# Kernel optimization log

Hardware: AMD Instinct MI355X
Metric: run time of the kernel (lower is better)

Reference implementation:

```python
import jax, jax.numpy as jnp
import numpy as np

B, N, D, E, K, C = 64, 32, 384, 8, 8, 1000  # batch, tokens, dim, experts, capacity, classes
KD = K * D   # expert_dims = 3072
ND = N * D   # 12288

def _gelu(v):
    return jax.nn.gelu(v, approximate=False)  # torch nn.GELU default = exact erf

def setup_inputs() -> dict:
    key = jax.random.key(0)
    ks = jax.random.split(key, 16)
    s = 0.02
    f = jnp.float32
    return {
        "x": jax.random.normal(ks[0], (B, N, D), f),
        "expert_emb": jax.random.normal(ks[1], (E, D), f) * s,
        "w1": jax.random.normal(ks[2], (E, KD, KD), f) * s,
        "b1": jnp.zeros((E, KD), f),
        "w2": jax.random.normal(ks[3], (E, KD, KD), f) * s,
        "b2": jnp.zeros((E, KD), f),
        "sw_w1": jax.random.normal(ks[4], (ND, ND), f) * s,
        "sw_b1": jnp.zeros((ND,), f),
        "sw_w2": jax.random.normal(ks[5], (ND, E), f) * s,
        "sw_b2": jnp.zeros((E,), f),
        "ch_w1": jax.random.normal(ks[6], (KD, KD), f) * s,
        "ch_b1": jnp.zeros((KD,), f),
        "ch_w2": jax.random.normal(ks[7], (KD, C), f) * s,
        "ch_b2": jnp.zeros((C,), f),
    }

def reference(x, expert_emb, w1, b1, w2, b2, sw_w1, sw_b1, sw_w2, sw_b2, ch_w1, ch_b1, ch_w2, ch_b2):
    # Router: scores (B, E, N), softmax over tokens, expert-choice top-k
    S = jax.nn.softmax(jnp.einsum('bnd,ed->ben', x, expert_emb), axis=2)
    G, I = jax.lax.top_k(S, K)  # (B, E, K); G is unused downstream (matches original)
    # Gather selected tokens per expert: (B, E, K, D)
    sel = x[jnp.arange(B)[:, None, None], I]
    sel = jnp.transpose(sel, (1, 0, 2, 3)).reshape(E, B, KD)  # e b (k d)
    # Per-expert MLP as grouped GEMM
    h = _gelu(jnp.einsum('ebi,eio->ebo', sel, w1) + b1[:, None, :])
    er = jnp.einsum('ebi,eio->ebo', h, w2) + b2[:, None, :]   # (E, B, KD)
    er = jnp.transpose(er, (1, 0, 2))                          # (B, E, KD)
    # Weighted combine: weights from Mlp over flattened input + softmax over experts
    xf = x.reshape(B, ND)
    w = jax.nn.softmax(_gelu(xf @ sw_w1 + sw_b1) @ sw_w2 + sw_b2, axis=1)  # (B, E)
    ws = jnp.einsum('bek,be->bk', er, w)                       # (B, KD)
    # Classification head
    return _gelu(ws @ ch_w1 + ch_b1) @ ch_w2 + ch_b2           # (B, C)
```

## Files before the change

kernel.cpp:

```cpp
#include <hip/hip_runtime.h>
#include <hip/hip_bf16.h>

using short8 = __attribute__((ext_vector_type(8))) short;
using f32x4  = __attribute__((ext_vector_type(4))) float;

typedef const __attribute__((address_space(1))) void* gvp;
typedef __attribute__((address_space(3))) void* lvp;

#define NB   64
#define NTOK 32
#define DD   384
#define NE   8
#define TK   8
#define NC   1000
#define KD   3072
#define ND   12288

__device__ __forceinline__ float gelu_f(float x) {
  return 0.5f * x * (1.0f + erff(x * 0.70710678118654752440f));
}

__device__ __forceinline__ unsigned short f2bf(float f) {
  unsigned u = __float_as_uint(f);
  u += 0x7fffu + ((u >> 16) & 1u);
  return (unsigned short)(u >> 16);
}

__global__ __launch_bounds__(256) void routing_kernel(
    const float* __restrict__ x, const float* __restrict__ emb,
    unsigned short* __restrict__ sel, unsigned short* __restrict__ xb)
{
  __shared__ float xs[NTOK][DD + 1];
  __shared__ float es[NE][DD + 1];
  __shared__ float lg[NE][NTOK];
  __shared__ int   Is[NE][TK];
  const int b = blockIdx.x, tid = threadIdx.x;

  for (int i = tid; i < NTOK * DD; i += 256) xs[i / DD][i % DD] = x[(size_t)b * ND + i];
  for (int i = tid; i < NE * DD;   i += 256) es[i / DD][i % DD] = emb[i];
  __syncthreads();

  {
    const int e = tid >> 5, n = tid & 31;
    float s = 0.f;
    for (int d = 0; d < DD; ++d) s += xs[n][d] * es[e][d];
    lg[e][n] = s;
  }
  __syncthreads();

  if (tid < NE) {
    const int e = tid;
    for (int k = 0; k < TK; ++k) {
      float best = lg[e][0]; int bi = 0;
      for (int n = 1; n < NTOK; ++n) { float v = lg[e][n]; if (v > best) { best = v; bi = n; } }
      Is[e][k] = bi;
      lg[e][bi] = -INFINITY;
    }
  }
  __syncthreads();

  for (int i = tid; i < NE * KD; i += 256) {
    const int e = i / KD, r = i % KD, k = r / DD, d = r % DD;
    const int n = Is[e][k];
    sel[((size_t)e * NB + b) * KD + r] = f2bf(xs[n][d]);
  }
  for (int i = tid; i < ND; i += 256) xb[(size_t)b * ND + i] = f2bf(xs[i / DD][i % DD]);
}

__device__ __forceinline__ void gemm_rt_body(
    const unsigned short* __restrict__ Ab, const float* __restrict__ Wz,
    float* __restrict__ op, const int K, const int N, const int NSTEP,
    const int n0, const int wv, const int lane, float* __restrict__ lw)
{
  const int srow = wv * 8 + (lane >> 5);
  const int scol = (((lane & 31) * 4) - wv * 8) & 127;
  const float* gsrc = Wz + (size_t)srow * N + n0 + scol;
  float* lbase = lw + wv * 1024 + lane * 4;

  auto stage = [&](int bf, int st) {
    const float* g = gsrc + (size_t)st * 32 * N;
    float* l = lbase + bf * 4096;
    #pragma unroll
    for (int r = 0; r < 4; ++r)
      __builtin_amdgcn_global_load_lds((gvp)(g + (size_t)(r * 2) * N),
                                       (lvp)(l + r * 256), 16, 0, 0);
  };

  const int ln = lane & 15, q = lane >> 4, g8 = q * 8;
  const unsigned short* ap = Ab + (size_t)ln * K + g8;
  const int colp0 = (wv * 32 +      ln + g8) & 127;
  const int colp1 = (wv * 32 + 16 + ln + g8) & 127;

  f32x4 acc[4][2];
  #pragma unroll
  for (int mt = 0; mt < 4; ++mt) {
    acc[mt][0] = (f32x4){0.f, 0.f, 0.f, 0.f};
    acc[mt][1] = (f32x4){0.f, 0.f, 0.f, 0.f};
  }

  stage(0, 0);
  for (int st = 0; st < NSTEP; ++st) {
    const int bf = st & 1;
    __syncthreads();
    if (st + 1 < NSTEP) stage(bf ^ 1, st + 1);

    const float* lb = lw + bf * 4096;
    union { short8 v; unsigned short u[8]; } pb0, pb1;
    #pragma unroll
    for (int j = 0; j < 8; ++j) {
      pb0.u[j] = f2bf(lb[(g8 + j) * 128 + colp0]);
      pb1.u[j] = f2bf(lb[(g8 + j) * 128 + colp1]);
    }
    #pragma unroll
    for (int mt = 0; mt < 4; ++mt) {
      const short8 afr = *reinterpret_cast<const short8*>(ap + (size_t)mt * 16 * K + st * 32);
      acc[mt][0] = __builtin_amdgcn_mfma_f32_16x16x32_bf16(afr, pb0.v, acc[mt][0], 0, 0, 0);
      acc[mt][1] = __builtin_amdgcn_mfma_f32_16x16x32_bf16(afr, pb1.v, acc[mt][1], 0, 0, 0);
    }
  }

  #pragma unroll
  for (int mt = 0; mt < 4; ++mt)
    #pragma unroll
    for (int s = 0; s < 2; ++s) {
      const int col = n0 + wv * 32 + s * 16 + ln;
      #pragma unroll
      for (int r = 0; r < 4; ++r)
        op[(size_t)(mt * 16 + q * 4 + r) * N + col] = acc[mt][s][r];
    }
}

template<int PHASE>
__global__ __launch_bounds__(256) void dual_gemm(
    const unsigned short* __restrict__ EA, const float* __restrict__ EW,
    float* __restrict__ EO,
    const unsigned short* __restrict__ xb, const float* __restrict__ sww1,
    float* __restrict__ tpt)
{
  __shared__ float lw[2][4096];
  const int t = threadIdx.x, wv = t >> 6, lane = t & 63;
  const int bid = blockIdx.x;
  const int grp = bid >> 1, rem = bid & 1;

  if (rem == 0) {
    const int idx = grp;
    const int z = idx & 1, bt = (idx >> 1) & 7, nx = idx >> 4;
    constexpr int KCH = KD / 2;
    gemm_rt_body(EA + (size_t)bt * 64 * KD + (size_t)z * KCH,
                 EW + (size_t)bt * KD * KD + (size_t)z * KCH * KD,
                 EO + ((size_t)z * NE + bt) * 64 * KD,
                 KD, KD, KCH / 32, nx * 128, wv, lane, &lw[0][0]);
  } else {
    const int idx = grp;
    const int z = PHASE * 4 + (idx & 3), nx = idx >> 2;
    constexpr int KCH = ND / 8;
    gemm_rt_body(xb + (size_t)z * KCH,
                 sww1 + (size_t)z * KCH * ND,
                 tpt + (size_t)z * 64 * ND,
                 ND, ND, KCH / 32, nx * 128, wv, lane, &lw[0][0]);
  }
}

template<int K, int N, int SPLIT, bool NGUARD>
__global__ __launch_bounds__(256) void gemm2(
    const unsigned short* __restrict__ A, const float* __restrict__ W,
    float* __restrict__ outp, const int nbatch)
{
  constexpr int KCH = K / SPLIT;
  constexpr int NSTEP = KCH / 32;
  __shared__ float lw[2][4096];

  const int t = threadIdx.x;
  const int wv = t >> 6, lane = t & 63;
  const int n0 = blockIdx.x * 128;
  const int bt = blockIdx.y, z = blockIdx.z;

  const unsigned short* Ab = A + (size_t)bt * 64 * K + (size_t)z * KCH;
  const float*          Wb = W + (size_t)bt * (size_t)K * N;

  const int srow = wv * 8 + (lane >> 5);
  const int scol = (((lane & 31) * 4) - wv * 8) & 127;
  const float* gsrc   = Wb + (size_t)(z * KCH + srow) * N + n0 + scol;
  const float* glimit = Wb + (size_t)K * N - 4;
  float* lbase = &lw[0][0] + wv * 1024 + lane * 4;

  auto stage = [&](int bf, int st) {
    const float* g = gsrc + (size_t)st * 32 * N;
    float* l = lbase + bf * 4096;
    #pragma unroll
    for (int r = 0; r < 4; ++r) {
      const float* gp = g + (size_t)(r * 2) * N;
      if (NGUARD && gp > glimit) gp = glimit;
      __builtin_amdgcn_global_load_lds((gvp)gp, (lvp)(l + r * 256), 16, 0, 0);
    }
  };

  const int ln = lane & 15, q = lane >> 4, g8 = q * 8;
  const unsigned short* ap = Ab + (size_t)ln * K + g8;
  const int colp0 = (wv * 32 +      ln + g8) & 127;
  const int colp1 = (wv * 32 + 16 + ln + g8) & 127;

  f32x4 acc[4][2];
  #pragma unroll
  for (int mt = 0; mt < 4; ++mt) {
    acc[mt][0] = (f32x4){0.f, 0.f, 0.f, 0.f};
    acc[mt][1] = (f32x4){0.f, 0.f, 0.f, 0.f};
  }

  stage(0, 0);
  for (int st = 0; st < NSTEP; ++st) {
    const int bf = st & 1;
    __syncthreads();
    if (st + 1 < NSTEP) stage(bf ^ 1, st + 1);

    const float* lb = &lw[bf][0];
    union { short8 v; unsigned short u[8]; } pb0, pb1;
    #pragma unroll
    for (int j = 0; j < 8; ++j) {
      pb0.u[j] = f2bf(lb[(g8 + j) * 128 + colp0]);
      pb1.u[j] = f2bf(lb[(g8 + j) * 128 + colp1]);
    }
    #pragma unroll
    for (int mt = 0; mt < 4; ++mt) {
      const short8 afr = *reinterpret_cast<const short8*>(ap + (size_t)mt * 16 * K + st * 32);
      acc[mt][0] = __builtin_amdgcn_mfma_f32_16x16x32_bf16(afr, pb0.v, acc[mt][0], 0, 0, 0);
      acc[mt][1] = __builtin_amdgcn_mfma_f32_16x16x32_bf16(afr, pb1.v, acc[mt][1], 0, 0, 0);
    }
  }

  float* op = outp + (size_t)(z * nbatch + bt) * 64 * N;
  #pragma unroll
  for (int mt = 0; mt < 4; ++mt)
    #pragma unroll
    for (int s = 0; s < 2; ++s) {
      const int col = n0 + wv * 32 + s * 16 + ln;
      if (NGUARD && col >= N) continue;
      #pragma unroll
      for (int r = 0; r < 4; ++r)
        op[(size_t)(mt * 16 + q * 4 + r) * N + col] = acc[mt][s][r];
    }
}

template<int SPLIT, bool GELU, bool OUTBF>
__global__ __launch_bounds__(256) void reduce_ep(
    const float* __restrict__ part, const float* __restrict__ bias,
    void* __restrict__ outv, const int N, const int nbatch)
{
  const int total = nbatch * 64 * N;
  const int idx = blockIdx.x * 256 + threadIdx.x;
  if (idx >= total) return;
  const int n = idx % N;
  const int bt = idx / (64 * N);
  float s = 0.f;
  #pragma unroll
  for (int zz = 0; zz < SPLIT; ++zz) s += part[(size_t)zz * total + idx];
  s += bias[(size_t)bt * N + n];
  if (GELU) s = gelu_f(s);
  if (OUTBF) ((unsigned short*)outv)[idx] = f2bf(s);
  else       ((float*)outv)[idx] = s;
}

__global__ __launch_bounds__(256) void sw1part_kernel(
    const float* __restrict__ tpt, const float* __restrict__ b1,
    const float* __restrict__ w2, float* __restrict__ pd)
{
  __shared__ float red[256][8];
  const int blk = blockIdx.x, tid = threadIdx.x;
  const int b = blk / 12, sl = blk % 12;
  const int base = sl * 1024;

  float p[8] = {0, 0, 0, 0, 0, 0, 0, 0};
  #pragma unroll
  for (int k = 0; k < 4; ++k) {
    const int i = base + k * 256 + tid;
    float tv = b1[i];
    #pragma unroll
    for (int zz = 0; zz < 8; ++zz)
      tv += tpt[(size_t)zz * (64 * ND) + (size_t)b * ND + i];
    tv = gelu_f(tv);
    const float4* wp = reinterpret_cast<const float4*>(w2 + (size_t)i * 8);
    const float4 wa = wp[0], wc = wp[1];
    p[0] += tv * wa.x; p[1] += tv * wa.y; p[2] += tv * wa.z; p[3] += tv * wa.w;
    p[4] += tv * wc.x; p[5] += tv * wc.y; p[6] += tv * wc.z; p[7] += tv * wc.w;
  }
  #pragma unroll
  for (int e = 0; e < 8; ++e) red[tid][e] = p[e];
  __syncthreads();
  for (int off = 128; off >= 1; off >>= 1) {
    if (tid < off) {
      #pragma unroll
      for (int e = 0; e < 8; ++e) red[tid][e] += red[tid + off][e];
    }
    __syncthreads();
  }
  if (tid < 8) pd[(size_t)blk * 8 + tid] = red[0][tid];
}

__global__ __launch_bounds__(256) void mix2s_kernel(
    const float* __restrict__ ep, const float* __restrict__ b2,
    const float* __restrict__ pd, const float* __restrict__ swb2,
    unsigned short* __restrict__ wsb)
{
  const int idx = blockIdx.x * 256 + threadIdx.x;
  const int b = idx / KD, c = idx % KD;

  float lg[8];
  #pragma unroll
  for (int e = 0; e < 8; ++e) lg[e] = swb2[e];
  for (int sl = 0; sl < 12; ++sl)
    #pragma unroll
    for (int e = 0; e < 8; ++e) lg[e] += pd[((size_t)b * 12 + sl) * 8 + e];
  float mx = lg[0];
  #pragma unroll
  for (int e = 1; e < 8; ++e) mx = fmaxf(mx, lg[e]);
  float sum = 0.f;
  float w[8];
  #pragma unroll
  for (int e = 0; e < 8; ++e) { w[e] = expf(lg[e] - mx); sum += w[e]; }
  const float inv = 1.f / sum;

  float s = 0.f;
  #pragma unroll
  for (int e = 0; e < NE; ++e) {
    float v = b2[(size_t)e * KD + c];
    #pragma unroll
    for (int zz = 0; zz < 2; ++zz)
      v += ep[((size_t)(zz * NE + e) * NB + b) * KD + c];
    s += v * (w[e] * inv);
  }
  wsb[idx] = f2bf(s);
}

extern "C" void kernel_launch(void* const* d_in, const int* in_sizes, int n_in,
                              void* d_out, int out_size, void* d_ws, size_t ws_size,
                              hipStream_t stream)
{
  (void)in_sizes; (void)n_in; (void)out_size; (void)ws_size;
  const float* x     = (const float*)d_in[0];
  const float* emb   = (const float*)d_in[1];
  const float* w1    = (const float*)d_in[2];
  const float* b1    = (const float*)d_in[3];
  const float* w2    = (const float*)d_in[4];
  const float* b2    = (const float*)d_in[5];
  const float* sw_w1 = (const float*)d_in[6];
  const float* sw_b1 = (const float*)d_in[7];
  const float* sw_w2 = (const float*)d_in[8];
  const float* sw_b2 = (const float*)d_in[9];
  const float* ch_w1 = (const float*)d_in[10];
  const float* ch_b1 = (const float*)d_in[11];
  const float* ch_w2 = (const float*)d_in[12];
  const float* ch_b2 = (const float*)d_in[13];
  float* out = (float*)d_out;

  char* ws = (char*)d_ws;
  size_t off = 0;
  auto alloc = [&](size_t bytes) -> void* {
    void* p = ws + off;
    off += (bytes + 255) & ~(size_t)255;
    return p;
  };
  unsigned short* sel  = (unsigned short*)alloc((size_t)NE * NB * KD * 2);
  unsigned short* xb   = (unsigned short*)alloc((size_t)NB * ND * 2);
  unsigned short* h    = (unsigned short*)alloc((size_t)NE * NB * KD * 2);
  float*          ep   = (float*)alloc((size_t)2 * NE * NB * KD * 4);
  float*          tpt  = (float*)alloc((size_t)8 * NB * ND * 4);
  float*          pd   = (float*)alloc((size_t)NB * 12 * 8 * 4);
  unsigned short* wsb  = (unsigned short*)alloc((size_t)NB * KD * 2);
  float*          g1p  = (float*)alloc((size_t)16 * NB * KD * 4);
  unsigned short* g1   = (unsigned short*)alloc((size_t)NB * KD * 2);
  float*          g2p  = (float*)alloc((size_t)32 * NB * NC * 4);

  routing_kernel<<<dim3(64), 256, 0, stream>>>(x, emb, sel, xb);
  dual_gemm<0><<<dim3(768), 256, 0, stream>>>(sel, w1, ep, xb, sw_w1, tpt);
  reduce_ep<2, true, true><<<dim3(6144), 256, 0, stream>>>(ep, b1, (void*)h, KD, 8);
  dual_gemm<1><<<dim3(768), 256, 0, stream>>>(h, w2, ep, xb, sw_w1, tpt);
  sw1part_kernel<<<dim3(768), 256, 0, stream>>>(tpt, sw_b1, sw_w2, pd);
  mix2s_kernel<<<dim3((NB * KD) / 256), 256, 0, stream>>>(ep, b2, pd, sw_b2, wsb);
  gemm2<KD, KD, 16, false><<<dim3(24, 1, 16), 256, 0, stream>>>(wsb, ch_w1, g1p, 1);
  reduce_ep<16, true, true><<<dim3(768), 256, 0, stream>>>(g1p, ch_b1, (void*)g1, KD, 1);
  gemm2<KD, NC, 32, true><<<dim3(8, 1, 32), 256, 0, stream>>>(g1, ch_w2, g2p, 1);
  reduce_ep<32, false, false><<<dim3((NB * NC + 255) / 256), 256, 0, stream>>>(g2p, ch_b2, (void*)out, NC, 1);
}
```

Baseline: 352.0 us.

## Fuse expert GEMM1 epilogue, move full sw_w1 GEMM into first pass, fold router MLP tail

```diff
diff --git a/kernel.cpp b/kernel.cpp
--- a/kernel.cpp
+++ b/kernel.cpp
@@ -67,10 +67,13 @@
   for (int i = tid; i < ND; i += 256) xb[(size_t)b * ND + i] = f2bf(xs[i / DD][i % DD]);
 }
 
+template<bool FUSED>
 __device__ __forceinline__ void gemm_rt_body(
     const unsigned short* __restrict__ Ab, const float* __restrict__ Wz,
-    float* __restrict__ op, const int K, const int N, const int NSTEP,
-    const int n0, const int wv, const int lane, float* __restrict__ lw)
+    const int K, const int N, const int NSTEP, const int n0,
+    const int wv, const int lane, float* __restrict__ lw,
+    float* __restrict__ opf, unsigned short* __restrict__ opb,
+    const float* __restrict__ bias)
 {
   const int srow = wv * 8 + (lane >> 5);
   const int scol = (((lane & 31) * 4) - wv * 8) & 127;
@@ -125,39 +128,97 @@
     for (int s = 0; s < 2; ++s) {
       const int col = n0 + wv * 32 + s * 16 + ln;
       #pragma unroll
-      for (int r = 0; r < 4; ++r)
-        op[(size_t)(mt * 16 + q * 4 + r) * N + col] = acc[mt][s][r];
-    }
-}
-
-template<int PHASE>
-__global__ __launch_bounds__(256) void dual_gemm(
-    const unsigned short* __restrict__ EA, const float* __restrict__ EW,
-    float* __restrict__ EO,
+      for (int r = 0; r < 4; ++r) {
+        const int row = mt * 16 + q * 4 + r;
+        if (FUSED) {
+          const float v = gelu_f(acc[mt][s][r] + bias[col]);
+          opb[(size_t)row * N + col] = f2bf(v);
+        } else {
+          opf[(size_t)row * N + col] = acc[mt][s][r];
+        }
+      }
+    }
+}
+
+__global__ __launch_bounds__(256) void dualA_kernel(
+    const unsigned short* __restrict__ sel, const float* __restrict__ w1,
+    const float* __restrict__ b1, unsigned short* __restrict__ h,
     const unsigned short* __restrict__ xb, const float* __restrict__ sww1,
     float* __restrict__ tpt)
 {
   __shared__ float lw[2][4096];
   const int t = threadIdx.x, wv = t >> 6, lane = t & 63;
   const int bid = blockIdx.x;
-  const int grp = bid >> 1, rem = bid & 1;
+  const int grp = bid / 3, rem = bid - grp * 3;
+
+  if (rem == 0) {
+    const int idx = grp;
+    const int bt = idx & 7, nx = idx >> 3;
+    gemm_rt_body<true>(sel + (size_t)bt * 64 * KD,
+                       w1 + (size_t)bt * KD * KD,
+                       KD, KD, KD / 32, nx * 128, wv, lane, &lw[0][0],
+                       nullptr, h + (size_t)bt * 64 * KD, b1 + (size_t)bt * KD);
+  } else {
+    const int idx = grp * 2 + (rem - 1);
+    const int z = idx & 3, nx = idx >> 2;
+    constexpr int KCH = ND / 4;
+    gemm_rt_body<false>(xb + (size_t)z * KCH,
+                        sww1 + (size_t)z * KCH * ND,
+                        ND, ND, KCH / 32, nx * 128, wv, lane, &lw[0][0],
+                        tpt + (size_t)z * 64 * ND, nullptr, nullptr);
+  }
+}
+
+__global__ __launch_bounds__(256) void dualB_kernel(
+    const unsigned short* __restrict__ h, const float* __restrict__ w2,
+    float* __restrict__ ep,
+    const float* __restrict__ tpt, const float* __restrict__ swb1,
+    const float* __restrict__ sww2, float* __restrict__ pd)
+{
+  __shared__ float lw[2][4096];
+  const int t = threadIdx.x, wv = t >> 6, lane = t & 63;
+  const int bid = blockIdx.x;
+  const int grp = bid / 3, rem = bid - grp * 3;
 
   if (rem == 0) {
     const int idx = grp;
     const int z = idx & 1, bt = (idx >> 1) & 7, nx = idx >> 4;
     constexpr int KCH = KD / 2;
-    gemm_rt_body(EA + (size_t)bt * 64 * KD + (size_t)z * KCH,
-                 EW + (size_t)bt * KD * KD + (size_t)z * KCH * KD,
-                 EO + ((size_t)z * NE + bt) * 64 * KD,
-                 KD, KD, KCH / 32, nx * 128, wv, lane, &lw[0][0]);
+    gemm_rt_body<false>(h + (size_t)bt * 64 * KD + (size_t)z * KCH,
+                        w2 + (size_t)bt * KD * KD + (size_t)z * KCH * KD,
+                        KD, KD, KCH / 32, nx * 128, wv, lane, &lw[0][0],
+                        ep + ((size_t)z * NE + bt) * 64 * KD, nullptr, nullptr);
   } else {
-    const int idx = grp;
-    const int z = PHASE * 4 + (idx & 3), nx = idx >> 2;
-    constexpr int KCH = ND / 8;
-    gemm_rt_body(xb + (size_t)z * KCH,
-                 sww1 + (size_t)z * KCH * ND,
-                 tpt + (size_t)z * 64 * ND,
-                 ND, ND, KCH / 32, nx * 128, wv, lane, &lw[0][0]);
+    const int idx = grp * 2 + (rem - 1);
+    const int b = idx / 12, sl = idx % 12;
+    const int base = sl * 1024;
+    float (*red)[8] = reinterpret_cast<float(*)[8]>(&lw[0][0]);
+
+    float p[8] = {0, 0, 0, 0, 0, 0, 0, 0};
+    #pragma unroll
+    for (int k = 0; k < 4; ++k) {
+      const int i = base + k * 256 + t;
+      float tv = swb1[i];
+      #pragma unroll
+      for (int zz = 0; zz < 4; ++zz)
+        tv += tpt[(size_t)zz * (64 * ND) + (size_t)b * ND + i];
+      tv = gelu_f(tv);
+      const float4* wp = reinterpret_cast<const float4*>(sww2 + (size_t)i * 8);
+      const float4 wa = wp[0], wc = wp[1];
+      p[0] += tv * wa.x; p[1] += tv * wa.y; p[2] += tv * wa.z; p[3] += tv * wa.w;
+      p[4] += tv * wc.x; p[5] += tv * wc.y; p[6] += tv * wc.z; p[7] += tv * wc.w;
+    }
+    #pragma unroll
+    for (int e = 0; e < 8; ++e) red[t][e] = p[e];
+    __syncthreads();
+    for (int off = 128; off >= 1; off >>= 1) {
+      if (t < off) {
+        #pragma unroll
+        for (int e = 0; e < 8; ++e) red[t][e] += red[t + off][e];
+      }
+      __syncthreads();
+    }
+    if (t < 8) pd[(size_t)idx * 8 + t] = red[0][t];
   }
 }
 
@@ -258,42 +319,6 @@
   if (GELU) s = gelu_f(s);
   if (OUTBF) ((unsigned short*)outv)[idx] = f2bf(s);
   else       ((float*)outv)[idx] = s;
-}
-
-__global__ __launch_bounds__(256) void sw1part_kernel(
-    const float* __restrict__ tpt, const float* __restrict__ b1,
-    const float* __restrict__ w2, float* __restrict__ pd)
-{
-  __shared__ float red[256][8];
-  const int blk = blockIdx.x, tid = threadIdx.x;
-  const int b = blk / 12, sl = blk % 12;
-  const int base = sl * 1024;
-
-  float p[8] = {0, 0, 0, 0, 0, 0, 0, 0};
-  #pragma unroll
-  for (int k = 0; k < 4; ++k) {
-    const int i = base + k * 256 + tid;
-    float tv = b1[i];
-    #pragma unroll
-    for (int zz = 0; zz < 8; ++zz)
-      tv += tpt[(size_t)zz * (64 * ND) + (size_t)b * ND + i];
-    tv = gelu_f(tv);
-    const float4* wp = reinterpret_cast<const float4*>(w2 + (size_t)i * 8);
-    const float4 wa = wp[0], wc = wp[1];
-    p[0] += tv * wa.x; p[1] += tv * wa.y; p[2] += tv * wa.z; p[3] += tv * wa.w;
-    p[4] += tv * wc.x; p[5] += tv * wc.y; p[6] += tv * wc.z; p[7] += tv * wc.w;
-  }
-  #pragma unroll
-  for (int e = 0; e < 8; ++e) red[tid][e] = p[e];
-  __syncthreads();
-  for (int off = 128; off >= 1; off >>= 1) {
-    if (tid < off) {
-      #pragma unroll
-      for (int e = 0; e < 8; ++e) red[tid][e] += red[tid + off][e];
-    }
-    __syncthreads();
-  }
-  if (tid < 8) pd[(size_t)blk * 8 + tid] = red[0][tid];
 }
 
 __global__ __launch_bounds__(256) void mix2s_kernel(
@@ -363,7 +388,7 @@
   unsigned short* xb   = (unsigned short*)alloc((size_t)NB * ND * 2);
   unsigned short* h    = (unsigned short*)alloc((size_t)NE * NB * KD * 2);
   float*          ep   = (float*)alloc((size_t)2 * NE * NB * KD * 4);
-  float*          tpt  = (float*)alloc((size_t)8 * NB * ND * 4);
+  float*          tpt  = (float*)alloc((size_t)4 * NB * ND * 4);
   float*          pd   = (float*)alloc((size_t)NB * 12 * 8 * 4);
   unsigned short* wsb  = (unsigned short*)alloc((size_t)NB * KD * 2);
   float*          g1p  = (float*)alloc((size_t)16 * NB * KD * 4);
@@ -371,10 +396,8 @@
   float*          g2p  = (float*)alloc((size_t)32 * NB * NC * 4);
 
   routing_kernel<<<dim3(64), 256, 0, stream>>>(x, emb, sel, xb);
-  dual_gemm<0><<<dim3(768), 256, 0, stream>>>(sel, w1, ep, xb, sw_w1, tpt);
-  reduce_ep<2, true, true><<<dim3(6144), 256, 0, stream>>>(ep, b1, (void*)h, KD, 8);
-  dual_gemm<1><<<dim3(768), 256, 0, stream>>>(h, w2, ep, xb, sw_w1, tpt);
-  sw1part_kernel<<<dim3(768), 256, 0, stream>>>(tpt, sw_b1, sw_w2, pd);
+  dualA_kernel<<<dim3(576), 256, 0, stream>>>(sel, w1, b1, h, xb, sw_w1, tpt);
+  dualB_kernel<<<dim3(1152), 256, 0, stream>>>(h, w2, ep, tpt, sw_b1, sw_w2, pd);
   mix2s_kernel<<<dim3((NB * KD) / 256), 256, 0, stream>>>(ep, b2, pd, sw_b2, wsb);
   gemm2<KD, KD, 16, false><<<dim3(24, 1, 16), 256, 0, stream>>>(wsb, ch_w1, g1p, 1);
   reduce_ep<16, true, true><<<dim3(768), 256, 0, stream>>>(g1p, ch_b1, (void*)g1, KD, 1);
```

Result: slower. 392.6 us (+11.5%).
